# Kernel tuning notes

Measured on AMD Instinct MI355X. Metric: run time of the kernel, lower is better.

Reference implementation:

```python
import jax, jax.numpy as jnp
import numpy as np

NEG_SLOPE = 0.2

def _gat_layer(x, src, dst, W, a_s, a_d, b, concat):
    # x: [N, F_in], W: [F_in, H*C], a_s/a_d: [H, C]
    N = x.shape[0]
    H, C = a_s.shape
    h = (x @ W).reshape(N, H, C)                       # per-head projection
    al_s = jnp.sum(h * a_s, axis=-1)                   # [N, H]
    al_d = jnp.sum(h * a_d, axis=-1)                   # [N, H]
    e = jax.nn.leaky_relu(al_s[src] + al_d[dst], NEG_SLOPE)  # [E, H]
    # segment softmax over incoming edges of each dst node
    m = jax.ops.segment_max(e, dst, num_segments=N)    # [N, H]
    ex = jnp.exp(e - m[dst])
    denom = jax.ops.segment_sum(ex, dst, num_segments=N)
    alpha = ex / denom[dst]                            # [E, H]
    msg = h[src] * alpha[:, :, None]                   # [E, H, C]
    out = jax.ops.segment_sum(msg, dst, num_segments=N)  # [N, H, C]
    if concat:
        return out.reshape(N, H * C) + b
    return out.mean(axis=1) + b


def setup_inputs() -> dict:
    key = jax.random.key(0)
    ks = jax.random.split(key, 12)
    N, F_in, H, C1, LAT, E = 16384, 512, 4, 128, 64, 262144
    x = jax.random.normal(ks[0], (N, F_in), dtype=jnp.float32)
    edge_index = jax.random.randint(ks[1], (2, E), 0, N, dtype=jnp.int64)
    s = 0.05
    return {
        'x': x,
        'edge_index': edge_index,
        'W1': jax.random.normal(ks[2], (F_in, H * C1), dtype=jnp.float32) * s,
        'a_src1': jax.random.normal(ks[3], (H, C1), dtype=jnp.float32) * s,
        'a_dst1': jax.random.normal(ks[4], (H, C1), dtype=jnp.float32) * s,
        'b1': jax.random.normal(ks[5], (H * C1,), dtype=jnp.float32) * s,
        'W2': jax.random.normal(ks[6], (H * C1, H * LAT), dtype=jnp.float32) * s,
        'a_src2': jax.random.normal(ks[7], (H, LAT), dtype=jnp.float32) * s,
        'a_dst2': jax.random.normal(ks[8], (H, LAT), dtype=jnp.float32) * s,
        'b2': jax.random.normal(ks[9], (LAT,), dtype=jnp.float32) * s,
    }


def reference(x, edge_index, W1, a_src1, a_dst1, b1, W2, a_src2, a_dst2, b2):
    N = x.shape[0]
    # PyG GATConv default add_self_loops=True
    loop = jnp.arange(N, dtype=edge_index.dtype)
    src = jnp.concatenate([edge_index[0], loop])
    dst = jnp.concatenate([edge_index[1], loop])
    h = jax.nn.relu(_gat_layer(x, src, dst, W1, a_src1, a_dst1, b1, concat=True))
    out = _gat_layer(h, src, dst, W2, a_src2, a_dst2, b2, concat=False)
    return out
```

## Files before the change

### kernel.cpp

```cpp
#include <hip/hip_runtime.h>
#include <stdint.h>
#include <stddef.h>
#include <limits.h>

typedef __bf16 bf16;
typedef __bf16 bf16x4 __attribute__((ext_vector_type(4)));
typedef __bf16 bf16x8 __attribute__((ext_vector_type(8)));
typedef float  f32x4  __attribute__((ext_vector_type(4)));

#define CAP 128

static __device__ __forceinline__ float lrelu(float x) { return x > 0.f ? x : 0.2f * x; }
static __device__ __forceinline__ float san(float v) { return (fabsf(v) < 1e4f) ? v : 0.0f; }
static __device__ __forceinline__ float wexp(float e) { return __expf(fminf(e, 30.f)); }

static __device__ __forceinline__ void async_load16(const bf16* g, bf16* l) {
  __builtin_amdgcn_global_load_lds((const __attribute__((address_space(1))) void*)g,
                                   (__attribute__((address_space(3))) void*)l, 16, 0, 0);
}

static __device__ __forceinline__ void drain_barrier() {
  asm volatile("s_waitcnt vmcnt(0) lgkmcnt(0)" ::: "memory");
  __builtin_amdgcn_s_barrier();
}


__global__ __launch_bounds__(256) void prep_w(int* __restrict__ cnt,
                                              const float* __restrict__ W1,
                                              const float* __restrict__ W2,
                                              bf16* __restrict__ W1T,
                                              bf16* __restrict__ W2T,
                                              int N) {
  int b = blockIdx.x;
  if (b < N / 256) { cnt[b * 256 + threadIdx.x] = 0; return; }
  b -= N / 256;
  __shared__ bf16 t[32][33];
  const float* in; bf16* out; int R, C, bx, by;
  if (b < 256) { in = W1; out = W1T; R = 512; C = 512; by = b >> 4; bx = b & 15; }
  else         { b -= 256; in = W2; out = W2T; R = 512; C = 256; by = b >> 3; bx = b & 7; }
  const int lane = threadIdx.x & 31, r8 = threadIdx.x >> 5;
#pragma unroll
  for (int k = 0; k < 4; ++k) {
    int r = by * 32 + r8 + k * 8, c = bx * 32 + lane;
    t[lane][r8 + k * 8] = (bf16)san(in[(size_t)r * C + c]);
  }
  __syncthreads();
#pragma unroll
  for (int k = 0; k < 4; ++k) {
    int oc = bx * 32 + r8 + k * 8;
    out[(size_t)oc * R + by * 32 + lane] = t[r8 + k * 8][lane];
  }
}


__global__ __launch_bounds__(256) void gemm_al_l1(const float* __restrict__ X,
                                                  const bf16* __restrict__ BT,
                                                  bf16* __restrict__ C,
                                                  const float* __restrict__ a_s,
                                                  const float* __restrict__ a_d,
                                                  float* __restrict__ al_s,
                                                  float* __restrict__ al_d,
                                                  const int* __restrict__ src,
                                                  const int* __restrict__ dst,
                                                  int E, int* __restrict__ cnt,
                                                  int* __restrict__ slots,
                                                  int M, int N, int K) {
  __shared__ __align__(16) bf16 As[2][64 * 32];
  __shared__ __align__(16) bf16 Bs[2][128 * 32];
  __shared__ float alred[2][64][2];
  const int tid = threadIdx.x;
  const int b   = blockIdx.x;

  if (b >= 1024) {
    for (int e = (b - 1024) * 256 + tid; e < E; e += 256 * 256) {
      int d = dst[e];
      int pos = atomicAdd(&cnt[d], 1);
      if (pos < CAP) slots[(size_t)d * CAP + pos] = src[e];
    }
    return;
  }

  const int lane = tid & 63;
  const int wave = tid >> 6;
  const int m0 = (b & 255) * 64;
  const int head = b >> 8;
  const int n0 = head * 128;
  const int wm = (wave >> 1) * 32;
  const int wn = (wave & 1) * 64;

  f32x4 acc[2][4] = {};

  const int id1 = tid + 256;
  const float* apx = X  + (size_t)(m0 + (tid >> 2)) * K + (tid & 3) * 8;
  const bf16*  b0p = BT + (size_t)(n0 + (tid >> 2)) * K + (tid & 3) * 8;
  const bf16*  b1p = BT + (size_t)(n0 + (id1 >> 2)) * K + (id1 & 3) * 8;

  const int kq = (lane >> 4) * 8;
  const int rA = wm + (lane & 15);
  const int rB = wn + (lane & 15);

  {
    async_load16(b0p, &Bs[0][tid * 8]);
    async_load16(b1p, &Bs[0][id1 * 8]);
    f32x4 u0 = *(const f32x4*)(apx);
    f32x4 u1 = *(const f32x4*)(apx + 4);
    bf16x8 w;
#pragma unroll
    for (int k = 0; k < 4; ++k) { w[k] = (bf16)san(u0[k]); w[4 + k] = (bf16)san(u1[k]); }
    *(bf16x8*)&As[0][tid * 8] = w;
    drain_barrier();
  }

  int cur = 0;
  for (int k0 = 0; k0 < K; k0 += 32) {
    const int kn = k0 + 32;
    const bool pf = (kn < K);
    f32x4 u0, u1;
    if (pf) {
      async_load16(b0p + kn, &Bs[cur ^ 1][tid * 8]);
      async_load16(b1p + kn, &Bs[cur ^ 1][id1 * 8]);
      u0 = *(const f32x4*)(apx + kn);
      u1 = *(const f32x4*)(apx + kn + 4);
    }

    bf16x8 af[2], bfv[4];
#pragma unroll
    for (int i = 0; i < 2; ++i) af[i]  = *(const bf16x8*)&As[cur][(rA + i * 16) * 32 + kq];
#pragma unroll
    for (int j = 0; j < 4; ++j) bfv[j] = *(const bf16x8*)&Bs[cur][(rB + j * 16) * 32 + kq];
#pragma unroll
    for (int i = 0; i < 2; ++i)
#pragma unroll
      for (int j = 0; j < 4; ++j)
        acc[i][j] = __builtin_amdgcn_mfma_f32_16x16x32_bf16(af[i], bfv[j], acc[i][j], 0, 0, 0);

    if (pf) {
      bf16x8 w;
#pragma unroll
      for (int k = 0; k < 4; ++k) { w[k] = (bf16)san(u0[k]); w[4 + k] = (bf16)san(u1[k]); }
      *(bf16x8*)&As[cur ^ 1][tid * 8] = w;
    }

    drain_barrier();
    cur ^= 1;
  }

  const int cc = lane & 15;
  const int rb = (lane >> 4) * 4;
#pragma unroll
  for (int i = 0; i < 2; ++i)
#pragma unroll
    for (int j = 0; j < 4; ++j) {
      int gcol = n0 + wn + j * 16 + cc;
#pragma unroll
      for (int r = 0; r < 4; ++r) {
        int grow = m0 + wm + i * 16 + rb + r;
        C[(size_t)grow * N + gcol] = (bf16)acc[i][j][r];
      }
    }

  {
    float asv[4], adv[4];
#pragma unroll
    for (int j = 0; j < 4; ++j) {
      int col = head * 128 + wn + j * 16 + cc;
      asv[j] = san(a_s[col]);
      adv[j] = san(a_d[col]);
    }
    const int wnh = wn >> 6;
#pragma unroll
    for (int i = 0; i < 2; ++i)
#pragma unroll
      for (int r = 0; r < 4; ++r) {
        float ps = 0.f, pd = 0.f;
#pragma unroll
        for (int j = 0; j < 4; ++j) { ps += acc[i][j][r] * asv[j]; pd += acc[i][j][r] * adv[j]; }
#pragma unroll
        for (int off = 1; off <= 8; off <<= 1) {
          ps += __shfl_xor(ps, off);
          pd += __shfl_xor(pd, off);
        }
        if (cc == 0) {
          int row = wm + i * 16 + rb + r;
          alred[wnh][row][0] = ps;
          alred[wnh][row][1] = pd;
        }
      }
    __syncthreads();
    if (tid < 64) {
      al_s[(size_t)(m0 + tid) * 4 + head] = alred[0][tid][0] + alred[1][tid][0];
      al_d[(size_t)(m0 + tid) * 4 + head] = alred[0][tid][1] + alred[1][tid][1];
    }
  }
}


__global__ __launch_bounds__(256) void gemm_al_l2(const bf16* __restrict__ A,
                                                  const bf16* __restrict__ BT,
                                                  bf16* __restrict__ C,
                                                  const float* __restrict__ a_s,
                                                  const float* __restrict__ a_d,
                                                  float* __restrict__ al_s,
                                                  float* __restrict__ al_d,
                                                  int M, int N, int K) {
  __shared__ __align__(16) bf16 As[2][64 * 32];
  __shared__ __align__(16) bf16 Bs[2][128 * 32];
  const int tid  = threadIdx.x;
  const int lane = tid & 63;
  const int wave = tid >> 6;
  const int m0 = blockIdx.x * 64;
  const int n0 = blockIdx.y * 128;
  const int wm = (wave >> 1) * 32;
  const int wn = (wave & 1) * 64;

  f32x4 acc[2][4] = {};

  const int tb = tid + 256;
  const bf16* ap  = A  + (size_t)(m0 + (tid >> 2)) * K + (tid & 3) * 8;
  const bf16* bp0 = BT + (size_t)(n0 + (tid >> 2)) * K + (tid & 3) * 8;
  const bf16* bp1 = BT + (size_t)(n0 + (tb  >> 2)) * K + (tb  & 3) * 8;

  const int kq = (lane >> 4) * 8;
  const int rA = wm + (lane & 15);
  const int rB = wn + (lane & 15);

  async_load16(ap,  &As[0][tid * 8]);
  async_load16(bp0, &Bs[0][tid * 8]);
  async_load16(bp1, &Bs[0][tb  * 8]);
  drain_barrier();

  int cur = 0;
  for (int k0 = 0; k0 < K; k0 += 32) {
    const int kn = k0 + 32;
    if (kn < K) {
      async_load16(ap  + kn, &As[cur ^ 1][tid * 8]);
      async_load16(bp0 + kn, &Bs[cur ^ 1][tid * 8]);
      async_load16(bp1 + kn, &Bs[cur ^ 1][tb  * 8]);
    }

    bf16x8 af[2], bfv[4];
#pragma unroll
    for (int i = 0; i < 2; ++i) af[i]  = *(const bf16x8*)&As[cur][(rA + i * 16) * 32 + kq];
#pragma unroll
    for (int j = 0; j < 4; ++j) bfv[j] = *(const bf16x8*)&Bs[cur][(rB + j * 16) * 32 + kq];
#pragma unroll
    for (int i = 0; i < 2; ++i)
#pragma unroll
      for (int j = 0; j < 4; ++j)
        acc[i][j] = __builtin_amdgcn_mfma_f32_16x16x32_bf16(af[i], bfv[j], acc[i][j], 0, 0, 0);

    drain_barrier();
    cur ^= 1;
  }

  const int cc = lane & 15;
  const int rb = (lane >> 4) * 4;
#pragma unroll
  for (int i = 0; i < 2; ++i)
#pragma unroll
    for (int j = 0; j < 4; ++j) {
      int gcol = n0 + wn + j * 16 + cc;
#pragma unroll
      for (int r = 0; r < 4; ++r) {
        int grow = m0 + wm + i * 16 + rb + r;
        C[(size_t)grow * N + gcol] = (bf16)acc[i][j][r];
      }
    }

  {
    const int head = blockIdx.y * 2 + (wn >> 6);
    float asv[4], adv[4];
#pragma unroll
    for (int j = 0; j < 4; ++j) {
      int col = head * 64 + j * 16 + cc;
      asv[j] = san(a_s[col]);
      adv[j] = san(a_d[col]);
    }
#pragma unroll
    for (int i = 0; i < 2; ++i)
#pragma unroll
      for (int r = 0; r < 4; ++r) {
        float ps = 0.f, pd = 0.f;
#pragma unroll
        for (int j = 0; j < 4; ++j) { ps += acc[i][j][r] * asv[j]; pd += acc[i][j][r] * adv[j]; }
#pragma unroll
        for (int off = 1; off <= 8; off <<= 1) {
          ps += __shfl_xor(ps, off);
          pd += __shfl_xor(pd, off);
        }
        if (cc == 0) {
          int row = m0 + wm + i * 16 + rb + r;
          al_s[(size_t)row * 4 + head] = ps;
          al_d[(size_t)row * 4 + head] = pd;
        }
      }
  }
}


__global__ __launch_bounds__(256) void sort_mkW(const float* __restrict__ al_s,
                                                const float* __restrict__ al_d,
                                                const int* __restrict__ cnt,
                                                int* __restrict__ slots,
                                                float* __restrict__ Linv,
                                                float* __restrict__ Wpl,
                                                float* __restrict__ Wself,
                                                int N) {
  const int wv   = threadIdx.x >> 6;
  const int lane = threadIdx.x & 63;
  const int n = blockIdx.x * 4 + wv;
  const int beg = n * CAP;
  const int len = min(cnt[n], CAP);
  const size_t plane = (size_t)N * CAP;
  const f32x4 alsn = *(const f32x4*)(al_s + (size_t)n * 4);
  const f32x4 aldn = *(const f32x4*)(al_d + (size_t)n * 4);

  f32x4 L = {0.f, 0.f, 0.f, 0.f};
  if (lane == 0) {
#pragma unroll
    for (int h = 0; h < 4; ++h) {
      float ws = wexp(lrelu(alsn[h] + aldn[h]));
      L[h] = ws;
      Wself[(size_t)h * N + n] = ws;
    }
  }

  if (len <= 64) {
    int v = (lane < len) ? slots[beg + lane] : INT_MAX;
    if (len > 1) {
#pragma unroll
      for (int k = 2; k <= 64; k <<= 1) {
#pragma unroll
        for (int j = k >> 1; j > 0; j >>= 1) {
          int p = __shfl_xor(v, j);
          bool take_min = (((lane & k) == 0) == ((lane & j) == 0));
          v = take_min ? min(v, p) : max(v, p);
        }
      }
      if (lane < len) slots[beg + lane] = v;
    }
    if (lane < len) {
      f32x4 a = *(const f32x4*)(al_s + (size_t)v * 4);
#pragma unroll
      for (int h = 0; h < 4; ++h) {
        float w = wexp(lrelu(a[h] + aldn[h]));
        L[h] += w;
        Wpl[(size_t)h * plane + beg + lane] = w;
      }
    }
  } else {
    if (lane == 0) {
      for (int i = beg + 1; i < beg + len; ++i) {
        int v = slots[i];
        int j = i - 1;
        while (j >= beg && slots[j] > v) { slots[j + 1] = slots[j]; --j; }
        slots[j + 1] = v;
      }
    }
    asm volatile("s_waitcnt vmcnt(0)" ::: "memory");
    for (int c0 = beg; c0 < beg + len; c0 += 64) {
      const int cl = min(64, beg + len - c0);
      if (lane < cl) {
        int s = slots[c0 + lane];
        f32x4 a = *(const f32x4*)(al_s + (size_t)s * 4);
#pragma unroll
        for (int h = 0; h < 4; ++h) {
          float w = wexp(lrelu(a[h] + aldn[h]));
          L[h] += w;
          Wpl[(size_t)h * plane + c0 + lane] = w;
        }
      }
    }
  }

  for (int off = 32; off; off >>= 1) {
#pragma unroll
    for (int h = 0; h < 4; ++h) L[h] += __shfl_xor(L[h], off);
  }
  if (lane == 0) {
    f32x4 o;
#pragma unroll
    for (int h = 0; h < 4; ++h) o[h] = 1.0f / L[h];
    *(f32x4*)(Linv + (size_t)n * 4) = o;
  }
}


__global__ __launch_bounds__(256) void aggregate1_x(const bf16* __restrict__ h1,
                                                    const int* __restrict__ cnt,
                                                    const int* __restrict__ slots,
                                                    const float* __restrict__ Wpl,
                                                    const float* __restrict__ Wself,
                                                    const float* __restrict__ Linv,
                                                    const float* __restrict__ bias,
                                                    bf16* __restrict__ out, int N) {
  const int sl   = blockIdx.x & 7;
  const int g    = blockIdx.x >> 3;
  const int wv   = threadIdx.x >> 6;
  const int lane = threadIdx.x & 63;
  const int n    = g * 4 + wv;
  const int hd   = sl >> 1;
  const int c8   = lane & 7;
  const int sub  = lane >> 3;
  const int cbase = sl * 64 + c8 * 8;
  const int beg = n * CAP;
  const int len = min(cnt[n], CAP);
  const float* wrow = Wpl + (size_t)hd * N * CAP + beg;

  float acc[8] = {};
  if (sub == 0) {
    float ws = Wself[(size_t)hd * N + n];
    bf16x8 hv = *(const bf16x8*)(h1 + (size_t)n * 512 + cbase);
#pragma unroll
    for (int k = 0; k < 8; ++k) acc[k] = ws * (float)hv[k];
  }

  for (int c0 = 0; c0 < len; c0 += 64) {
    const int cl = min(64, len - c0);
    int   v = (lane < cl) ? slots[beg + c0 + lane] : 0;
    float w = (lane < cl) ? wrow[c0 + lane] : 0.f;
    for (int j0 = 0; j0 < cl; j0 += 8) {
      int jj = j0 + sub;
      int   sj = __shfl(v, jj);
      float wj = __shfl(w, jj);
      bf16x8 rv = *(const bf16x8*)(h1 + (size_t)sj * 512 + cbase);
#pragma unroll
      for (int k = 0; k < 8; ++k) acc[k] += wj * (float)rv[k];
    }
  }

#pragma unroll
  for (int off = 8; off <= 32; off <<= 1)
#pragma unroll
    for (int k = 0; k < 8; ++k) acc[k] += __shfl_xor(acc[k], off);

  if (sub == 0) {
    const float inv = Linv[(size_t)n * 4 + hd];
    bf16x8 ov;
#pragma unroll
    for (int k = 0; k < 8; ++k)
      ov[k] = (bf16)fmaxf(acc[k] * inv + san(bias[cbase + k]), 0.f);
    *(bf16x8*)(out + (size_t)n * 512 + cbase) = ov;
  }
}


__global__ __launch_bounds__(256) void aggregate2_f(const bf16* __restrict__ h2,
                                                    const float* __restrict__ al_s,
                                                    const float* __restrict__ al_d,
                                                    const int* __restrict__ cnt,
                                                    const int* __restrict__ slots,
                                                    const float* __restrict__ bias,
                                                    float* __restrict__ out) {
  __shared__ int   sIdx[4][64];
  __shared__ f32x4 sW[4][64];
  const int wv   = threadIdx.x >> 6;
  const int lane = threadIdx.x & 63;
  const int n = blockIdx.x * 4 + wv;
  const int hd = lane >> 4;
  const int cb = lane * 4;
  const int beg = n * CAP;
  const int len = min(cnt[n], CAP);
  const f32x4 alsn = *(const f32x4*)(al_s + (size_t)n * 4);
  const f32x4 aldn = *(const f32x4*)(al_d + (size_t)n * 4);

  const float wself = wexp(lrelu(alsn[hd] + aldn[hd]));
  bf16x4 hv0 = *(const bf16x4*)(h2 + (size_t)n * 256 + cb);
  float acc0 = wself * (float)hv0[0], acc1 = wself * (float)hv0[1];
  float acc2 = wself * (float)hv0[2], acc3 = wself * (float)hv0[3];
  f32x4 Lv = {0.f, 0.f, 0.f, 0.f};
  if (lane == 0) {
#pragma unroll
    for (int h = 0; h < 4; ++h) Lv[h] = wexp(lrelu(alsn[h] + aldn[h]));
  }
  for (int c0 = beg; c0 < beg + len; c0 += 64) {
    const int cl = min(64, beg + len - c0);
    if (lane < cl) {
      int s = slots[c0 + lane];
      sIdx[wv][lane] = s;
      f32x4 a = *(const f32x4*)(al_s + (size_t)s * 4);
      f32x4 w;
#pragma unroll
      for (int h = 0; h < 4; ++h) w[h] = wexp(lrelu(a[h] + aldn[h]));
      sW[wv][lane] = w;
#pragma unroll
      for (int h = 0; h < 4; ++h) Lv[h] += w[h];
    }
#pragma unroll 4
    for (int j = 0; j < cl; ++j) {
      int s = sIdx[wv][j];
      float a = sW[wv][j][hd];
      bf16x4 hv = *(const bf16x4*)(h2 + (size_t)s * 256 + cb);
      acc0 += a * (float)hv[0];
      acc1 += a * (float)hv[1];
      acc2 += a * (float)hv[2];
      acc3 += a * (float)hv[3];
    }
  }
  for (int off = 32; off; off >>= 1) {
#pragma unroll
    for (int h = 0; h < 4; ++h) Lv[h] += __shfl_xor(Lv[h], off);
  }
  const float inv = 1.0f / Lv[hd];
  acc0 *= inv; acc1 *= inv; acc2 *= inv; acc3 *= inv;
  acc0 += __shfl_xor(acc0, 16); acc1 += __shfl_xor(acc1, 16);
  acc2 += __shfl_xor(acc2, 16); acc3 += __shfl_xor(acc3, 16);
  acc0 += __shfl_xor(acc0, 32); acc1 += __shfl_xor(acc1, 32);
  acc2 += __shfl_xor(acc2, 32); acc3 += __shfl_xor(acc3, 32);
  if (lane < 16) {
    int ob = lane * 4;
    f32x4 ov;
    ov[0] = 0.25f * acc0 + san(bias[ob]);
    ov[1] = 0.25f * acc1 + san(bias[ob + 1]);
    ov[2] = 0.25f * acc2 + san(bias[ob + 2]);
    ov[3] = 0.25f * acc3 + san(bias[ob + 3]);
    *(f32x4*)(out + (size_t)n * 64 + ob) = ov;
  }
}


extern "C" void kernel_launch(void* const* d_in, const int* in_sizes, int n_in,
                              void* d_out, int out_size, void* d_ws, size_t ws_size,
                              hipStream_t stream) {
  const float* x   = (const float*)d_in[0];
  const int*   ei  = (const int*)d_in[1];
  const float* W1  = (const float*)d_in[2];
  const float* as1 = (const float*)d_in[3];
  const float* ad1 = (const float*)d_in[4];
  const float* b1  = (const float*)d_in[5];
  const float* W2  = (const float*)d_in[6];
  const float* as2 = (const float*)d_in[7];
  const float* ad2 = (const float*)d_in[8];
  const float* b2  = (const float*)d_in[9];
  float* outp = (float*)d_out;

  const int N = in_sizes[0] / 512;
  const int E = in_sizes[1] / 2;
  const int* src = ei;
  const int* dst = ei + E;

  char* p = (char*)d_ws;
  auto alloc = [&](size_t bytes) {
    char* r = p;
    p += (bytes + 255) & ~(size_t)255;
    return r;
  };
  bf16* h1    = (bf16*)alloc((size_t)N * 512 * 2);
  bf16* hbuf  = (bf16*)alloc((size_t)N * 512 * 2);
  bf16* W1T   = (bf16*)alloc((size_t)512 * 512 * 2);
  bf16* W2T   = (bf16*)alloc((size_t)256 * 512 * 2);
  float* al_s1 = (float*)alloc((size_t)N * 4 * 4);
  float* al_d1 = (float*)alloc((size_t)N * 4 * 4);
  float* al_s2 = (float*)alloc((size_t)N * 4 * 4);
  float* al_d2 = (float*)alloc((size_t)N * 4 * 4);
  float* Linv1 = (float*)alloc((size_t)N * 4 * 4);
  int* cnt     = (int*)alloc((size_t)N * 4);
  int* slots   = (int*)alloc((size_t)N * CAP * 4);
  float* Wpl   = (float*)alloc((size_t)4 * N * CAP * 4);
  float* Wself = (float*)alloc((size_t)4 * N * 4);
  bf16* h2 = h1;

  prep_w<<<N / 256 + 256 + 128, 256, 0, stream>>>(cnt, W1, W2, W1T, W2T, N);

  gemm_al_l1<<<1024 + 256, 256, 0, stream>>>(x, W1T, h1, as1, ad1, al_s1, al_d1,
                                             src, dst, E, cnt, slots, N, 512, 512);
  sort_mkW<<<N / 4, 256, 0, stream>>>(al_s1, al_d1, cnt, slots, Linv1, Wpl, Wself, N);
  aggregate1_x<<<8 * (N / 4), 256, 0, stream>>>(h1, cnt, slots, Wpl, Wself, Linv1,
                                                b1, hbuf, N);

  gemm_al_l2<<<dim3(N / 64, 2), 256, 0, stream>>>(hbuf, W2T, h2, as2, ad2, al_s2, al_d2,
                                                  N, 256, 512);
  aggregate2_f<<<N / 4, 256, 0, stream>>>(h2, al_s2, al_d2, cnt, slots, b2, outp);
}
```

Before: 212.8 us.

## Map eight destination nodes per wave in layer-1 aggregation instead of one

The layer-1 aggregation kernel now gives each 8-lane group its own destination node, so one wave covers eight nodes rather than splitting one node's edge list across eight sub-groups. This removes the per-chunk shuffles of slot indices and weights and the final cross-lane reduction, and cuts the grid size by eight. In exchange, each group walks its edge list serially up to the longest list in the wave, so imbalanced degrees leave lanes idle. Lanes in a group also read the same slot and weight values redundantly.

```diff
diff --git a/kernel.cpp b/kernel.cpp
--- a/kernel.cpp
+++ b/kernel.cpp
@@ -386,7 +386,7 @@
 }
 
 
-__global__ __launch_bounds__(256) void aggregate1_x(const bf16* __restrict__ h1,
+__global__ __launch_bounds__(256) void aggregate1_n(const bf16* __restrict__ h1,
                                                     const int* __restrict__ cnt,
                                                     const int* __restrict__ slots,
                                                     const float* __restrict__ Wpl,
@@ -398,50 +398,44 @@
   const int g    = blockIdx.x >> 3;
   const int wv   = threadIdx.x >> 6;
   const int lane = threadIdx.x & 63;
-  const int n    = g * 4 + wv;
+  const int nb   = lane >> 3;
+  const int c8   = lane & 7;
+  const int n    = g * 32 + wv * 8 + nb;
   const int hd   = sl >> 1;
-  const int c8   = lane & 7;
-  const int sub  = lane >> 3;
   const int cbase = sl * 64 + c8 * 8;
-  const int beg = n * CAP;
-  const int len = min(cnt[n], CAP);
+  const int beg  = n * CAP;
+  const int len  = min(cnt[n], CAP);
   const float* wrow = Wpl + (size_t)hd * N * CAP + beg;
-
-  float acc[8] = {};
-  if (sub == 0) {
-    float ws = Wself[(size_t)hd * N + n];
+  const int*   srow = slots + beg;
+
+  int ml = len;
+#pragma unroll
+  for (int off = 8; off <= 32; off <<= 1) ml = max(ml, __shfl_xor(ml, off));
+
+  float acc[8];
+  {
+    const float ws = Wself[(size_t)hd * N + n];
     bf16x8 hv = *(const bf16x8*)(h1 + (size_t)n * 512 + cbase);
 #pragma unroll
     for (int k = 0; k < 8; ++k) acc[k] = ws * (float)hv[k];
   }
 
-  for (int c0 = 0; c0 < len; c0 += 64) {
-    const int cl = min(64, len - c0);
-    int   v = (lane < cl) ? slots[beg + c0 + lane] : 0;
-    float w = (lane < cl) ? wrow[c0 + lane] : 0.f;
-    for (int j0 = 0; j0 < cl; j0 += 8) {
-      int jj = j0 + sub;
-      int   sj = __shfl(v, jj);
-      float wj = __shfl(w, jj);
-      bf16x8 rv = *(const bf16x8*)(h1 + (size_t)sj * 512 + cbase);
-#pragma unroll
-      for (int k = 0; k < 8; ++k) acc[k] += wj * (float)rv[k];
-    }
-  }
-
-#pragma unroll
-  for (int off = 8; off <= 32; off <<= 1)
-#pragma unroll
-    for (int k = 0; k < 8; ++k) acc[k] += __shfl_xor(acc[k], off);
-
-  if (sub == 0) {
-    const float inv = Linv[(size_t)n * 4 + hd];
-    bf16x8 ov;
-#pragma unroll
-    for (int k = 0; k < 8; ++k)
-      ov[k] = (bf16)fmaxf(acc[k] * inv + san(bias[cbase + k]), 0.f);
-    *(bf16x8*)(out + (size_t)n * 512 + cbase) = ov;
-  }
+#pragma unroll 4
+  for (int j = 0; j < ml; ++j) {
+    const bool ok = (j < len);
+    int   s = ok ? srow[j] : 0;
+    float w = ok ? wrow[j] : 0.f;
+    bf16x8 rv = *(const bf16x8*)(h1 + (size_t)s * 512 + cbase);
+#pragma unroll
+    for (int k = 0; k < 8; ++k) acc[k] += w * (float)rv[k];
+  }
+
+  const float inv = Linv[(size_t)n * 4 + hd];
+  bf16x8 ov;
+#pragma unroll
+  for (int k = 0; k < 8; ++k)
+    ov[k] = (bf16)fmaxf(acc[k] * inv + san(bias[cbase + k]), 0.f);
+  *(bf16x8*)(out + (size_t)n * 512 + cbase) = ov;
 }
 
 
@@ -565,8 +559,8 @@
   gemm_al_l1<<<1024 + 256, 256, 0, stream>>>(x, W1T, h1, as1, ad1, al_s1, al_d1,
                                              src, dst, E, cnt, slots, N, 512, 512);
   sort_mkW<<<N / 4, 256, 0, stream>>>(al_s1, al_d1, cnt, slots, Linv1, Wpl, Wself, N);
-  aggregate1_x<<<8 * (N / 4), 256, 0, stream>>>(h1, cnt, slots, Wpl, Wself, Linv1,
-                                                b1, hbuf, N);
+  aggregate1_n<<<8 * (N / 32), 256, 0, stream>>>(h1, cnt, slots, Wpl, Wself, Linv1,
+                                                 b1, hbuf, N);
 
   gemm_al_l2<<<dim3(N / 64, 2), 256, 0, stream>>>(hbuf, W2T, h2, as2, ad2, al_s2, al_d2,
                                                   N, 256, 512);
```

Result: faster. 202.9 us (-4.7%).
